# Kernel optimization log

Measured on AMD Instinct MI355X. Metric: run time of the kernel, lower is better.

The kernel has to match this reference:

```python
import jax, jax.numpy as jnp
import numpy as np

B, D, H, E = 1024, 2048, 2048, 16
K = 8            # args.topk
ENERGY_T = 1.0   # args.energy_T
EXP_ID = 0       # args.id (anchor expert)
DROP = 0.2       # hard-coded dropout_coefficient
KEEP = int(K * (1.0 - DROP))  # 6


def setup_inputs() -> dict:
    key = jax.random.key(0)
    ks = jax.random.split(key, 5)
    x = jax.random.normal(ks[0], (B, D), dtype=jnp.float32)
    Wg = jax.random.normal(ks[1], (D, E), dtype=jnp.float32) * 0.02
    bg = jnp.zeros((E,), dtype=jnp.float32)
    We = jax.random.normal(ks[2], (E, D, H), dtype=jnp.float32) * 0.02
    be = jnp.zeros((E, H), dtype=jnp.float32)
    return {"x": x, "Wg": Wg, "bg": bg, "We": We, "be": be}


def reference(x, Wg, bg, We, be):
    # gating: softmax over experts, then top-k (sorted descending, as torch.topk)
    gate = jax.nn.softmax(x @ Wg + bg, axis=-1)          # [B, E]
    vals, idx = jax.lax.top_k(gate, K)                   # [B, K]

    # all expert outputs (E is small; cheaper than gathering [B,K,D,H] weights)
    out_all = jnp.einsum('bd,edh->beh', x, We) + be      # [B, E, H]
    out_k = jnp.take_along_axis(out_all, idx[:, :, None], axis=1)  # [B, K, H]

    # elementwise cosine similarity vs. anchor expert output
    rep = out_all[:, EXP_ID]                             # [B, H]
    cos = (rep[:, None, :] * out_k) / (
        jnp.abs(rep)[:, None, :] * jnp.abs(out_k) + 1e-8)
    cos = jnp.where((idx == EXP_ID)[:, :, None], 1.0, cos)

    # energy/confidence H_k = T * logsumexp(cos / T) over feature dim
    energy = ENERGY_T * jax.nn.logsumexp(cos / ENERGY_T, axis=-1)  # [B, K]

    # keep the KEEP lowest-energy experts (stable sort, as python list.sort)
    keep_pos = jnp.argsort(energy, axis=-1)[:, :KEEP]    # [B, KEEP]
    vals_kept = jnp.take_along_axis(vals, keep_pos, axis=1)           # [B, KEEP]
    out_kept = jnp.take_along_axis(out_k, keep_pos[:, :, None], axis=1)  # [B, KEEP, H]

    return jnp.sum(vals_kept[:, :, None] * out_kept, axis=1)  # [B, H]
```

## Files before the change

### kernel.cpp

```cpp
#include <hip/hip_runtime.h>
#include <math.h>

#define B_ 1024
#define D_ 2048
#define H_ 2048
#define E_ 16
#define K_ 8
#define KEEP_ 6
#define EXP_ID_ 0

typedef double v4d __attribute__((ext_vector_type(4)));

#define WS_OUTALL 0
#define WS_IDX    134217728
#define WS_VALS   (134217728 + 32768)
#define WS_ENERGY (134217728 + 65536)
#define WS_CNT    (134217728 + 98304)
#define WS_ROWS   (134217728 + 98560)
#define WS_ROWTAB (134217728 + 164096)
#define WS_COLTAB (134217728 + 165120)
#define WS_OKFLG  (134217728 + 166144)

__global__ void init_cnt_kernel(int* __restrict__ cnt, int* __restrict__ okflg) {
  if (threadIdx.x < E_) cnt[threadIdx.x] = 0;
  if (threadIdx.x == 0) okflg[0] = 1;
}

__global__ __launch_bounds__(64) void mfma_probe_kernel(
    int* __restrict__ rowtab, int* __restrict__ coltab, int* __restrict__ okflg) {
  const int l = threadIdx.x;
  const v4d z = {0.0, 0.0, 0.0, 0.0};
  double a1 = (double)(l & 15);
  double b1 = ((l >> 4) == 0) ? 1.0 : 0.0;
  v4d d1 = __builtin_amdgcn_mfma_f64_16x16x4f64(a1, b1, z, 0, 0, 0);
  double a2 = ((l >> 4) == 0) ? 1.0 : 0.0;
  double b2 = (double)(l & 15);
  v4d d2 = __builtin_amdgcn_mfma_f64_16x16x4f64(a2, b2, z, 0, 0, 0);
  double a3 = (double)((l & 15) + 1);
  double b3 = (double)((l & 15) + 1);
  v4d d3 = __builtin_amdgcn_mfma_f64_16x16x4f64(a3, b3, z, 0, 0, 0);

  int ok = 1;
#pragma unroll
  for (int g = 0; g < 4; ++g) {
    int r = (int)(d1[g] + 0.5);
    int c = (int)(d2[g] + 0.5);
    if (r < 0 || r > 15 || c < 0 || c > 15) { r = 0; c = 0; ok = 0; }
    rowtab[l * 4 + g] = r;
    coltab[l * 4 + g] = c;
    double expect = 4.0 * (double)(r + 1) * (double)(c + 1);
    if (d3[g] != expect) ok = 0;
  }
  if (!ok) okflg[0] = 0;
}

__global__ __launch_bounds__(64) void gate_kernel(
    const float* __restrict__ x, const float* __restrict__ Wg,
    const float* __restrict__ bg, int* __restrict__ idx, float* __restrict__ vals,
    int* __restrict__ cnt, int* __restrict__ rows) {
  const int b = blockIdx.x;
  const int lane = threadIdx.x;
  double acc[E_];
#pragma unroll
  for (int e = 0; e < E_; ++e) acc[e] = 0.0;
  for (int d = lane; d < D_; d += 64) {
    double xv = (double)x[(size_t)b * D_ + d];
    const float* w = Wg + (size_t)d * E_;
#pragma unroll
    for (int e = 0; e < E_; ++e) acc[e] = fma(xv, (double)w[e], acc[e]);
  }
  for (int off = 32; off > 0; off >>= 1) {
#pragma unroll
    for (int e = 0; e < E_; ++e) acc[e] += __shfl_down(acc[e], off, 64);
  }
  if (lane == 0) {
    double logit[E_];
#pragma unroll
    for (int e = 0; e < E_; ++e) logit[e] = acc[e] + (double)bg[e];
    double m = logit[0];
#pragma unroll
    for (int e = 1; e < E_; ++e) m = fmax(m, logit[e]);
    double p[E_], s = 0.0;
#pragma unroll
    for (int e = 0; e < E_; ++e) { p[e] = exp(logit[e] - m); s += p[e]; }
#pragma unroll
    for (int e = 0; e < E_; ++e) p[e] = p[e] / s;
    unsigned taken = 0;
    for (int j = 0; j < K_; ++j) {
      int best = -1; double bv = -1.0;
#pragma unroll
      for (int e = 0; e < E_; ++e)
        if (!((taken >> e) & 1u) && p[e] > bv) { bv = p[e]; best = e; }
      taken |= (1u << best);
      idx[b * K_ + j] = best;
      vals[b * K_ + j] = (float)bv;
    }
    taken |= 1u;
#pragma unroll
    for (int e = 0; e < E_; ++e) {
      if ((taken >> e) & 1u) {
        int p2 = atomicAdd(&cnt[e], 1);
        rows[e * B_ + p2] = b;
      }
    }
  }
}

#define BM 64
#define BN 64
#define BK 16

__global__ __launch_bounds__(256) void gemm_expert_kernel(
    const float* __restrict__ X, const float* __restrict__ We,
    const float* __restrict__ be, float* __restrict__ out_all,
    const int* __restrict__ cnt, const int* __restrict__ rows,
    const int* __restrict__ rowtab, const int* __restrict__ coltab) {
  const int e  = blockIdx.z;
  const int nrows = cnt[e];
  const int m0 = blockIdx.y * BM;
  if (m0 >= nrows) return;
  const int n0 = blockIdx.x * BN;
  const float* Bmat = We + (size_t)e * D_ * H_;
  const int* rl = rows + e * B_;

  __shared__ float As[2][BM][BK + 4];
  __shared__ float Bs[2][BK][BN + 8];

  const int tid = threadIdx.x;
  const int arow  = tid >> 2;
  const int acol4 = (tid & 3) * 4;
  const int brow  = tid >> 4;
  const int bcol4 = (tid & 15) * 4;

  const int gidx = m0 + arow;
  const int grow = rl[(gidx < nrows) ? gidx : (nrows - 1)];
  const float* aptr = X + (size_t)grow * D_;
  const float* bptr = Bmat + (size_t)brow * H_ + n0 + bcol4;

  const int lane = tid & 63;
  const int wave = tid >> 6;
  const int lr = lane & 15;
  const int lq = lane >> 4;

  v4d acc[4];
#pragma unroll
  for (int c = 0; c < 4; ++c) acc[c] = (v4d){0.0, 0.0, 0.0, 0.0};

  float4 av = *(const float4*)(aptr + acol4);
  float4 bv = *(const float4*)(bptr);
  *(float4*)&As[0][arow][acol4] = av;
  *(float4*)&Bs[0][brow][bcol4] = bv;

#define COMPUTE_TILE(BUF)                                                    \
  _Pragma("unroll")                                                          \
  for (int k4 = 0; k4 < BK; k4 += 4) {                                       \
    double a = (double)As[BUF][wave * 16 + lr][k4 + lq];                     \
    _Pragma("unroll")                                                        \
    for (int c = 0; c < 4; ++c) {                                            \
      double bb = (double)Bs[BUF][k4 + lq][c * 16 + lr];                     \
      acc[c] = __builtin_amdgcn_mfma_f64_16x16x4f64(a, bb, acc[c], 0, 0, 0); \
    }                                                                        \
  }

  for (int k0 = 0; k0 < D_; k0 += 2 * BK) {
    __syncthreads();
    av = *(const float4*)(aptr + (k0 + BK) + acol4);
    bv = *(const float4*)(bptr + (size_t)(k0 + BK) * H_);
    COMPUTE_TILE(0)
    *(float4*)&As[1][arow][acol4] = av;
    *(float4*)&Bs[1][brow][bcol4] = bv;
    __syncthreads();
    const bool more = (k0 + 2 * BK) < D_;
    if (more) {
      av = *(const float4*)(aptr + (k0 + 2 * BK) + acol4);
      bv = *(const float4*)(bptr + (size_t)(k0 + 2 * BK) * H_);
    }
    COMPUTE_TILE(1)
    if (more) {
      *(float4*)&As[0][arow][acol4] = av;
      *(float4*)&Bs[0][brow][bcol4] = bv;
    }
  }
#undef COMPUTE_TILE

  int drow[4], dcol[4];
#pragma unroll
  for (int g = 0; g < 4; ++g) {
    drow[g] = rowtab[lane * 4 + g];
    dcol[g] = coltab[lane * 4 + g];
  }
#pragma unroll
  for (int c = 0; c < 4; ++c) {
#pragma unroll
    for (int g = 0; g < 4; ++g) {
      const int rix = m0 + wave * 16 + drow[g];
      if (rix < nrows) {
        const int mrow = rl[rix];
        const int col = n0 + c * 16 + dcol[g];
        out_all[((size_t)mrow * E_ + e) * H_ + col] =
            (float)(acc[c][g] + (double)be[(size_t)e * H_ + col]);
      }
    }
  }
}

__global__ __launch_bounds__(256) void energy_kernel(
    const float* __restrict__ out_all, const int* __restrict__ idx,
    float* __restrict__ energy) {
  const int b = blockIdx.x, j = blockIdx.y, t = threadIdx.x;
  const int e = idx[b * K_ + j];
  if (e == EXP_ID_) {
    if (t == 0) energy[b * K_ + j] = 1.0f + (float)log(2048.0);
    return;
  }
  const float* rep = out_all + ((size_t)b * E_ + EXP_ID_) * H_;
  const float* ok  = out_all + ((size_t)b * E_ + e) * H_;

  __shared__ float cs[H_];
  __shared__ float red[256];
  __shared__ float chain[128];

  float mx = -2.0f;
  for (int h = t; h < H_; h += 256) {
    float r = rep[h], o = ok[h];
    float num = r * o;
    float den = fabsf(r) * fabsf(o) + 1e-8f;
    float c = num / den;
    cs[h] = c;
    mx = fmaxf(mx, c);
  }
  red[t] = mx;
  __syncthreads();
  for (int off = 128; off > 0; off >>= 1) {
    if (t < off) red[t] = fmaxf(red[t], red[t + off]);
    __syncthreads();
  }
  const float m = red[0];
  __syncthreads();

  if (t < 128) {
    const int blk = t >> 3, jj = t & 7;
    const float* base = cs + blk * 128;
    float d0 = base[jj] - m;
    float r = (float)exp((double)d0);
#pragma unroll
    for (int q = 1; q < 16; ++q) {
      float dq = base[q * 8 + jj] - m;
      float term = (float)exp((double)dq);
      r = r + term;
    }
    chain[t] = r;
  }
  __syncthreads();

  if (t == 0) {
    float Bsum[16];
#pragma unroll
    for (int blk = 0; blk < 16; ++blk) {
      const float* c8 = chain + blk * 8;
      float s01 = c8[0] + c8[1];
      float s23 = c8[2] + c8[3];
      float s45 = c8[4] + c8[5];
      float s67 = c8[6] + c8[7];
      Bsum[blk] = (s01 + s23) + (s45 + s67);
    }
    float C[8], D[4], Ee[2];
#pragma unroll
    for (int i = 0; i < 8; ++i) C[i] = Bsum[2 * i] + Bsum[2 * i + 1];
#pragma unroll
    for (int i = 0; i < 4; ++i) D[i] = C[2 * i] + C[2 * i + 1];
#pragma unroll
    for (int i = 0; i < 2; ++i) Ee[i] = D[2 * i] + D[2 * i + 1];
    float S = Ee[0] + Ee[1];
    energy[b * K_ + j] = m + (float)log((double)S);
  }
}

__global__ __launch_bounds__(256) void final_kernel(
    const float* __restrict__ out_all, const int* __restrict__ idx,
    const float* __restrict__ vals, const float* __restrict__ energy,
    float* __restrict__ out) {
  const int b = blockIdx.x;
  const int h = blockIdx.y * 256 + threadIdx.x;
  float En[K_];
#pragma unroll
  for (int j = 0; j < K_; ++j) En[j] = energy[b * K_ + j];
  double s = 0.0;
#pragma unroll
  for (int j = 0; j < K_; ++j) {
    int pos = 0;
#pragma unroll
    for (int j2 = 0; j2 < K_; ++j2)
      pos += (En[j2] < En[j]) || (En[j2] == En[j] && j2 < j);
    if (pos < KEEP_) {
      int e = idx[b * K_ + j];
      s += (double)vals[b * K_ + j] *
           (double)out_all[((size_t)b * E_ + e) * H_ + h];
    }
  }
  out[(size_t)b * H_ + h] = (float)s;
}

extern "C" void kernel_launch(void* const* d_in, const int* in_sizes, int n_in,
                              void* d_out, int out_size, void* d_ws, size_t ws_size,
                              hipStream_t stream) {
  const float* x  = (const float*)d_in[0];
  const float* Wg = (const float*)d_in[1];
  const float* bg = (const float*)d_in[2];
  const float* We = (const float*)d_in[3];
  const float* be = (const float*)d_in[4];
  float* out = (float*)d_out;

  char* ws = (char*)d_ws;
  float* out_all = (float*)(ws + WS_OUTALL);
  int*   idx     = (int*)(ws + WS_IDX);
  float* vals    = (float*)(ws + WS_VALS);
  float* energy  = (float*)(ws + WS_ENERGY);
  int*   cnt     = (int*)(ws + WS_CNT);
  int*   rows    = (int*)(ws + WS_ROWS);
  int*   rowtab  = (int*)(ws + WS_ROWTAB);
  int*   coltab  = (int*)(ws + WS_COLTAB);
  int*   okflg   = (int*)(ws + WS_OKFLG);

  init_cnt_kernel<<<dim3(1), dim3(64), 0, stream>>>(cnt, okflg);

  mfma_probe_kernel<<<dim3(1), dim3(64), 0, stream>>>(rowtab, coltab, okflg);

  gate_kernel<<<dim3(B_), dim3(64), 0, stream>>>(x, Wg, bg, idx, vals, cnt, rows);

  gemm_expert_kernel<<<dim3(H_ / BN, B_ / BM, E_), dim3(256), 0, stream>>>(
      x, We, be, out_all, cnt, rows, rowtab, coltab);

  energy_kernel<<<dim3(B_, K_), dim3(256), 0, stream>>>(out_all, idx, energy);

  final_kernel<<<dim3(B_, H_ / 256), dim3(256), 0, stream>>>(
      out_all, idx, vals, energy, out);
}
```

Baseline: 1.469 ms.

## Load A operand directly into registers and double BK for expert GEMM

The A tile no longer goes through shared memory. Each lane loads the strided X elements it needs for the FP64 MFMA straight from global memory into registers, double-buffered with prefetch. BK grows from 16 to 32, which halves the number of barriers per K and adds a second B row per thread. The aim is to cut LDS traffic and synchronisation, at the cost of uncoalesced scalar global loads of X (stride 4 floats per lane) and higher register pressure.

```diff
diff --git a/kernel.cpp b/kernel.cpp
--- a/kernel.cpp
+++ b/kernel.cpp
@@ -108,7 +108,7 @@
 
 #define BM 64
 #define BN 64
-#define BK 16
+#define BK 32
 
 __global__ __launch_bounds__(256) void gemm_expert_kernel(
     const float* __restrict__ X, const float* __restrict__ We,
@@ -123,18 +123,12 @@
   const float* Bmat = We + (size_t)e * D_ * H_;
   const int* rl = rows + e * B_;
 
-  __shared__ float As[2][BM][BK + 4];
   __shared__ float Bs[2][BK][BN + 8];
 
   const int tid = threadIdx.x;
-  const int arow  = tid >> 2;
-  const int acol4 = (tid & 3) * 4;
   const int brow  = tid >> 4;
   const int bcol4 = (tid & 15) * 4;
 
-  const int gidx = m0 + arow;
-  const int grow = rl[(gidx < nrows) ? gidx : (nrows - 1)];
-  const float* aptr = X + (size_t)grow * D_;
   const float* bptr = Bmat + (size_t)brow * H_ + n0 + bcol4;
 
   const int lane = tid & 63;
@@ -142,43 +136,57 @@
   const int lr = lane & 15;
   const int lq = lane >> 4;
 
+  const int aidx = m0 + wave * 16 + lr;
+  const int agrow = rl[(aidx < nrows) ? aidx : (nrows - 1)];
+  const float* arow = X + (size_t)agrow * D_;
+
   v4d acc[4];
 #pragma unroll
   for (int c = 0; c < 4; ++c) acc[c] = (v4d){0.0, 0.0, 0.0, 0.0};
 
-  float4 av = *(const float4*)(aptr + acol4);
-  float4 bv = *(const float4*)(bptr);
-  *(float4*)&As[0][arow][acol4] = av;
-  *(float4*)&Bs[0][brow][bcol4] = bv;
+  float4 bva = *(const float4*)(bptr);
+  float4 bvb = *(const float4*)(bptr + (size_t)16 * H_);
+  *(float4*)&Bs[0][brow][bcol4] = bva;
+  *(float4*)&Bs[0][brow + 16][bcol4] = bvb;
+  float a[8], na[8];
+#pragma unroll
+  for (int i = 0; i < 8; ++i) a[i] = arow[lq + 4 * i];
 
 #define COMPUTE_TILE(BUF)                                                    \
   _Pragma("unroll")                                                          \
-  for (int k4 = 0; k4 < BK; k4 += 4) {                                       \
-    double a = (double)As[BUF][wave * 16 + lr][k4 + lq];                     \
+  for (int i = 0; i < 8; ++i) {                                              \
+    double a_ = (double)a[i];                                                \
     _Pragma("unroll")                                                        \
-    for (int c = 0; c < 4; ++c) {                                            \
-      double bb = (double)Bs[BUF][k4 + lq][c * 16 + lr];                     \
-      acc[c] = __builtin_amdgcn_mfma_f64_16x16x4f64(a, bb, acc[c], 0, 0, 0); \
-    }                                                                        \
+    for (int c = 0; c < 4; ++c)                                              \
+      acc[c] = __builtin_amdgcn_mfma_f64_16x16x4f64(                         \
+          a_, (double)Bs[BUF][4 * i + lq][c * 16 + lr], acc[c], 0, 0, 0);    \
   }
 
   for (int k0 = 0; k0 < D_; k0 += 2 * BK) {
     __syncthreads();
-    av = *(const float4*)(aptr + (k0 + BK) + acol4);
-    bv = *(const float4*)(bptr + (size_t)(k0 + BK) * H_);
+    bva = *(const float4*)(bptr + (size_t)(k0 + BK) * H_);
+    bvb = *(const float4*)(bptr + (size_t)(k0 + BK + 16) * H_);
+#pragma unroll
+    for (int i = 0; i < 8; ++i) na[i] = arow[k0 + BK + lq + 4 * i];
     COMPUTE_TILE(0)
-    *(float4*)&As[1][arow][acol4] = av;
-    *(float4*)&Bs[1][brow][bcol4] = bv;
+    *(float4*)&Bs[1][brow][bcol4] = bva;
+    *(float4*)&Bs[1][brow + 16][bcol4] = bvb;
+#pragma unroll
+    for (int i = 0; i < 8; ++i) a[i] = na[i];
     __syncthreads();
     const bool more = (k0 + 2 * BK) < D_;
     if (more) {
-      av = *(const float4*)(aptr + (k0 + 2 * BK) + acol4);
-      bv = *(const float4*)(bptr + (size_t)(k0 + 2 * BK) * H_);
+      bva = *(const float4*)(bptr + (size_t)(k0 + 2 * BK) * H_);
+      bvb = *(const float4*)(bptr + (size_t)(k0 + 2 * BK + 16) * H_);
+#pragma unroll
+      for (int i = 0; i < 8; ++i) na[i] = arow[k0 + 2 * BK + lq + 4 * i];
     }
     COMPUTE_TILE(1)
     if (more) {
-      *(float4*)&As[0][arow][acol4] = av;
-      *(float4*)&Bs[0][brow][bcol4] = bv;
+      *(float4*)&Bs[0][brow][bcol4] = bva;
+      *(float4*)&Bs[0][brow + 16][bcol4] = bvb;
+#pragma unroll
+      for (int i = 0; i < 8; ++i) a[i] = na[i];
     }
   }
 #undef COMPUTE_TILE
```

After: 1.479 ms. Within noise of the previous version (+0.7%).
